# Kernel tuning notes

Hardware: AMD Instinct MI355X
Metric: run time of the kernel (lower is better)

Reference implementation:

```python
import jax, jax.numpy as jnp
import numpy as np

WS = 8          # window size
N = WS * WS     # tokens per window
H = 4           # num heads
DIM = 128
HD = DIM // H   # head dim
SCALE = HD ** -0.5


def _rel_pos_index(ws):
    coords = np.stack(np.meshgrid(np.arange(ws), np.arange(ws), indexing='ij')).reshape(2, -1)
    rel = coords[:, :, None] - coords[:, None, :]          # [2, N, N]
    rel = rel.transpose(1, 2, 0)                           # [N, N, 2]
    rel[..., 0] += ws - 1
    rel[..., 1] += ws - 1
    rel[..., 0] *= 2 * ws - 1
    return jnp.asarray(rel.sum(-1), dtype=jnp.int32)       # [N, N]

_REL_IDX = _rel_pos_index(WS)


def setup_inputs() -> dict:
    key = jax.random.key(0)
    ks = jax.random.split(key, 7)
    B_ = 8192
    nW = 64
    return {
        'x': jax.random.normal(ks[0], (B_, N, DIM), dtype=jnp.float32),
        'mask': jax.random.normal(ks[1], (nW, N, N), dtype=jnp.float32),
        'qkv_w': jax.random.normal(ks[2], (3 * DIM, DIM), dtype=jnp.float32) * 0.02,
        'qkv_b': jax.random.normal(ks[3], (3 * DIM,), dtype=jnp.float32) * 0.02,
        'proj_w': jax.random.normal(ks[4], (DIM, DIM), dtype=jnp.float32) * 0.02,
        'proj_b': jax.random.normal(ks[5], (DIM,), dtype=jnp.float32) * 0.02,
        'rel_pos_bias': jax.random.normal(ks[6], ((2 * WS - 1) ** 2, H), dtype=jnp.float32) * 0.02,
    }


def reference(x, mask, qkv_w, qkv_b, proj_w, proj_b, rel_pos_bias):
    B_, n, c = x.shape
    nW = mask.shape[0]
    qkv = x @ qkv_w.T + qkv_b                               # [B_, N, 3C]
    qkv = qkv.reshape(B_, n, 3, H, HD).transpose(2, 0, 3, 1, 4)
    q, k, v = qkv[0], qkv[1], qkv[2]                        # [B_, H, N, HD]
    attn = jnp.einsum('bhnd,bhmd->bhnm', q * SCALE, k)      # [B_, H, N, N]
    bias = rel_pos_bias[_REL_IDX.reshape(-1)].reshape(n, n, H)
    attn = attn + bias.transpose(2, 0, 1)[None]
    attn = attn.reshape(B_ // nW, nW, H, n, n) + mask[None, :, None, :, :]
    attn = attn.reshape(B_, H, n, n)
    attn = jax.nn.softmax(attn, axis=-1)
    out = jnp.einsum('bhnm,bhmd->bnhd', attn, v).reshape(B_, n, c)
    return out @ proj_w.T + proj_b
```

## Files before the change

### kernel.cpp

```cpp
#include <hip/hip_runtime.h>
#include <stdint.h>

typedef __attribute__((ext_vector_type(8))) short short8;
typedef __attribute__((ext_vector_type(4))) float f32x4;

#define SCALE_Q 0.17677669529663687f

__device__ __forceinline__ uint16_t f2bf(float f) {
    uint32_t u = __builtin_bit_cast(uint32_t, f);
    u += 0x7FFFu + ((u >> 16) & 1u);
    return (uint16_t)(u >> 16);
}

__global__ void prep_kernel(const float* __restrict__ qkv_w, const float* __restrict__ qkv_b,
                            const float* __restrict__ proj_w, const float* __restrict__ rel_b,
                            uint16_t* __restrict__ wq, float* __restrict__ bq,
                            uint16_t* __restrict__ wp, float* __restrict__ bT) {
    int t = blockIdx.x * 256 + threadIdx.x;
    if (t < 384 * 128) {
        int o = t >> 7;
        float s = (o < 128) ? SCALE_Q : 1.0f;
        wq[t] = f2bf(qkv_w[t] * s);
    }
    if (t < 384) bq[t] = qkv_b[t] * ((t < 128) ? SCALE_Q : 1.0f);
    if (t < 128 * 128) wp[t] = f2bf(proj_w[t]);
    if (t < 4 * 64 * 64) {
        int h = t & 3, nm = t >> 2, n = nm >> 6, m = nm & 63;
        int idx = ((n >> 3) - (m >> 3) + 7) * 15 + ((n & 7) - (m & 7) + 7);
        bT[(h * 64 + n) * 64 + m] = rel_b[idx * 4 + h];
    }
}

__global__ __launch_bounds__(256, 2) void winattn_kernel(
    const float* __restrict__ x, const float* __restrict__ mask,
    const uint16_t* __restrict__ wq, const float* __restrict__ bq,
    const uint16_t* __restrict__ wp, const float* __restrict__ pb,
    const float* __restrict__ bT, float* __restrict__ out)
{
    __shared__ uint16_t regionA[20480];
    __shared__ uint16_t Vs[4][64][32];

    uint16_t* Qs = regionA;
    uint16_t* Ks = regionA + 4*64*40;
    uint16_t* Ps = regionA;
    uint16_t* Os = regionA;

    const int b    = blockIdx.x;
    const int w    = b & 63;
    const int wid  = threadIdx.x >> 6;
    const int lane = threadIdx.x & 63;
    const int l15  = lane & 15;
    const int lg   = lane >> 4;

    short8 xa[4][4];
    const float* xb = x + (size_t)b * (64 * 128);
    #pragma unroll
    for (int rt = 0; rt < 4; ++rt) {
      #pragma unroll
      for (int ks = 0; ks < 4; ++ks) {
        const float* p = xb + (rt*16 + l15)*128 + ks*32 + lg*8;
        f32x4 f0 = *(const f32x4*)p;
        f32x4 f1 = *(const f32x4*)(p + 4);
        short8 a;
        a[0]=(short)f2bf(f0[0]); a[1]=(short)f2bf(f0[1]); a[2]=(short)f2bf(f0[2]); a[3]=(short)f2bf(f0[3]);
        a[4]=(short)f2bf(f1[0]); a[5]=(short)f2bf(f1[1]); a[6]=(short)f2bf(f1[2]); a[7]=(short)f2bf(f1[3]);
        xa[rt][ks] = a;
      }
    }
    #pragma unroll
    for (int ct = 0; ct < 6; ++ct) {
        const int obase = wid*96 + ct*16;
        short8 wb[4];
        #pragma unroll
        for (int ks = 0; ks < 4; ++ks)
            wb[ks] = *(const short8*)(wq + (obase + l15)*128 + ks*32 + lg*8);
        const int o   = obase + l15;
        const int sec = o >> 7;
        const int hh  = (o >> 5) & 3;
        const int d   = o & 31;
        const float bo = bq[o];
        const int stride = (sec == 2) ? 32 : 40;
        uint16_t* dst = (sec == 0) ? (Qs + hh*64*40 + d)
                       : (sec == 1) ? (Ks + hh*64*40 + d)
                       : (&Vs[0][0][0] + hh*64*32 + d);
        #pragma unroll
        for (int rt = 0; rt < 4; ++rt) {
            f32x4 acc = {0.f, 0.f, 0.f, 0.f};
            #pragma unroll
            for (int ks = 0; ks < 4; ++ks)
                acc = __builtin_amdgcn_mfma_f32_16x16x32_bf16(xa[rt][ks], wb[ks], acc, 0, 0, 0);
            #pragma unroll
            for (int r = 0; r < 4; ++r)
                dst[(rt*16 + lg*4 + r) * stride] = f2bf(acc[r] + bo);
        }
    }
    __syncthreads();

    const int h = wid;
    short8 qf[4], kf[4];
    #pragma unroll
    for (int rt = 0; rt < 4; ++rt)
        qf[rt] = *(const short8*)(Qs + (h*64 + rt*16 + l15)*40 + lg*8);
    #pragma unroll
    for (int ct = 0; ct < 4; ++ct)
        kf[ct] = *(const short8*)(Ks + (h*64 + ct*16 + l15)*40 + lg*8);
    f32x4 sacc[4][4];
    #pragma unroll
    for (int rt = 0; rt < 4; ++rt) {
      #pragma unroll
      for (int ct = 0; ct < 4; ++ct) {
        f32x4 z = {0.f, 0.f, 0.f, 0.f};
        sacc[rt][ct] = __builtin_amdgcn_mfma_f32_16x16x32_bf16(qf[rt], kf[ct], z, 0, 0, 0);
      }
    }
    const float* bTh = bT + h*64*64;
    const float* mkw = mask + w*64*64;
    float rcp[4][4];
    #pragma unroll
    for (int rt = 0; rt < 4; ++rt) {
      #pragma unroll
      for (int r = 0; r < 4; ++r) {
        const int row = rt*16 + lg*4 + r;
        float v[4];
        #pragma unroll
        for (int ct = 0; ct < 4; ++ct) {
            const int col = ct*16 + l15;
            v[ct] = sacc[rt][ct][r] + bTh[row*64 + col] + mkw[row*64 + col];
        }
        float mx = fmaxf(fmaxf(v[0], v[1]), fmaxf(v[2], v[3]));
        mx = fmaxf(mx, __shfl_xor(mx, 1));
        mx = fmaxf(mx, __shfl_xor(mx, 2));
        mx = fmaxf(mx, __shfl_xor(mx, 4));
        mx = fmaxf(mx, __shfl_xor(mx, 8));
        float s = 0.f;
        #pragma unroll
        for (int ct = 0; ct < 4; ++ct) {
            v[ct] = __expf(v[ct] - mx);
            s += v[ct];
            sacc[rt][ct][r] = v[ct];
        }
        s += __shfl_xor(s, 1);
        s += __shfl_xor(s, 2);
        s += __shfl_xor(s, 4);
        s += __shfl_xor(s, 8);
        rcp[rt][r] = 1.0f / s;
      }
    }
    __syncthreads();
    #pragma unroll
    for (int rt = 0; rt < 4; ++rt)
      #pragma unroll
      for (int ct = 0; ct < 4; ++ct)
        #pragma unroll
        for (int r = 0; r < 4; ++r)
            Ps[(h*64 + rt*16 + lg*4 + r)*80 + ct*16 + l15] = f2bf(sacc[rt][ct][r]);
    __syncthreads();

    short8 pf[4][2];
    #pragma unroll
    for (int rt = 0; rt < 4; ++rt)
      #pragma unroll
      for (int ks = 0; ks < 2; ++ks)
        pf[rt][ks] = *(const short8*)(Ps + (h*64 + rt*16 + l15)*80 + ks*32 + lg*8);
    short8 vf[2][2];
    #pragma unroll
    for (int ks = 0; ks < 2; ++ks) {
      #pragma unroll
      for (int c2 = 0; c2 < 2; ++c2) {
        short8 vv;
        #pragma unroll
        for (int e = 0; e < 8; ++e)
            vv[e] = (short)Vs[h][ks*32 + lg*8 + e][c2*16 + l15];
        vf[ks][c2] = vv;
      }
    }
    f32x4 oacc[4][2];
    #pragma unroll
    for (int rt = 0; rt < 4; ++rt) {
      #pragma unroll
      for (int c2 = 0; c2 < 2; ++c2) {
        f32x4 acc = {0.f, 0.f, 0.f, 0.f};
        #pragma unroll
        for (int ks = 0; ks < 2; ++ks)
            acc = __builtin_amdgcn_mfma_f32_16x16x32_bf16(pf[rt][ks], vf[ks][c2], acc, 0, 0, 0);
        oacc[rt][c2] = acc;
      }
    }
    __syncthreads();
    #pragma unroll
    for (int rt = 0; rt < 4; ++rt)
      #pragma unroll
      for (int c2 = 0; c2 < 2; ++c2)
        #pragma unroll
        for (int r = 0; r < 4; ++r)
            Os[(rt*16 + lg*4 + r)*136 + h*32 + c2*16 + l15] = f2bf(oacc[rt][c2][r] * rcp[rt][r]);
    __syncthreads();

    short8 of[4][4];
    #pragma unroll
    for (int rt = 0; rt < 4; ++rt)
      #pragma unroll
      for (int ks = 0; ks < 4; ++ks)
        of[rt][ks] = *(const short8*)(Os + (rt*16 + l15)*136 + ks*32 + lg*8);
    float* outb = out + (size_t)b * (64 * 128);
    #pragma unroll
    for (int ct = 0; ct < 2; ++ct) {
        const int c = wid*32 + ct*16 + l15;
        short8 pwf[4];
        #pragma unroll
        for (int ks = 0; ks < 4; ++ks)
            pwf[ks] = *(const short8*)(wp + c*128 + ks*32 + lg*8);
        const float pbias = pb[c];
        #pragma unroll
        for (int rt = 0; rt < 4; ++rt) {
            f32x4 acc = {0.f, 0.f, 0.f, 0.f};
            #pragma unroll
            for (int ks = 0; ks < 4; ++ks)
                acc = __builtin_amdgcn_mfma_f32_16x16x32_bf16(of[rt][ks], pwf[ks], acc, 0, 0, 0);
            #pragma unroll
            for (int r = 0; r < 4; ++r)
                outb[(rt*16 + lg*4 + r)*128 + c] = acc[r] + pbias;
        }
    }
}

extern "C" void kernel_launch(void* const* d_in, const int* in_sizes, int n_in,
                              void* d_out, int out_size, void* d_ws, size_t ws_size,
                              hipStream_t stream) {
    const float* x      = (const float*)d_in[0];
    const float* mask   = (const float*)d_in[1];
    const float* qkv_w  = (const float*)d_in[2];
    const float* qkv_b  = (const float*)d_in[3];
    const float* proj_w = (const float*)d_in[4];
    const float* proj_b = (const float*)d_in[5];
    const float* rel_b  = (const float*)d_in[6];
    float* out = (float*)d_out;

    char* ws = (char*)d_ws;
    uint16_t* wq = (uint16_t*)ws;
    float*    bq = (float*)(ws + 98304);
    uint16_t* wp = (uint16_t*)(ws + 99840);
    float*    bT = (float*)(ws + 132608);

    const int B_ = in_sizes[0] / (64 * 128);

    hipLaunchKernelGGL(prep_kernel, dim3(192), dim3(256), 0, stream,
                       qkv_w, qkv_b, proj_w, rel_b, wq, bq, wp, bT);
    hipLaunchKernelGGL(winattn_kernel, dim3(B_), dim3(256), 0, stream,
                       x, mask, wq, bq, wp, proj_b, bT, out);
}
```

Before: 360.5 us.

## Restructure window attention kernel with transposed MFMA layouts, exp2 softmax and register-resident P

Reworks the fused window-attention kernel. The QKV GEMM now uses a swapped operand order so each lane writes packed bf16 vectors, with V stored transposed. Scores are computed as K·Q^T so softmax reductions need only two cross-lane shuffles and bias/mask are read as float4. P stays in registers for the PV MFMA instead of round-tripping through LDS. It also folds log2e into the Q scale and bias to use exp2f and a hardware reciprocal, uses v_cvt_pk_bf16_f32 for packed conversion, and shrinks shared memory with launch bounds raised to 3 blocks per CU. The extra occupancy target may cost registers or cause spills.

Result: slower. 386.2 us (+7.1%).

```diff
diff --git a/kernel.cpp b/kernel.cpp
--- a/kernel.cpp
+++ b/kernel.cpp
@@ -2,8 +2,12 @@
 #include <stdint.h>
 
 typedef __attribute__((ext_vector_type(8))) short short8;
+typedef __attribute__((ext_vector_type(4))) short s16x4;
 typedef __attribute__((ext_vector_type(4))) float f32x4;
-
+typedef __attribute__((ext_vector_type(4))) uint32_t u32x4;
+typedef __attribute__((ext_vector_type(2))) uint32_t u32x2;
+
+#define LOG2E   1.4426950408889634f
 #define SCALE_Q 0.17677669529663687f
 
 __device__ __forceinline__ uint16_t f2bf(float f) {
@@ -12,38 +16,39 @@
     return (uint16_t)(u >> 16);
 }
 
+__device__ __forceinline__ uint32_t cvtpk(float a, float b) {
+    uint32_t r;
+    asm("v_cvt_pk_bf16_f32 %0, %1, %2" : "=v"(r) : "v"(a), "v"(b));
+    return r;
+}
+
 __global__ void prep_kernel(const float* __restrict__ qkv_w, const float* __restrict__ qkv_b,
                             const float* __restrict__ proj_w, const float* __restrict__ rel_b,
                             uint16_t* __restrict__ wq, float* __restrict__ bq,
-                            uint16_t* __restrict__ wp, float* __restrict__ bT) {
+                            uint16_t* __restrict__ wp, float* __restrict__ bTs) {
     int t = blockIdx.x * 256 + threadIdx.x;
     if (t < 384 * 128) {
         int o = t >> 7;
-        float s = (o < 128) ? SCALE_Q : 1.0f;
+        float s = (o < 128) ? SCALE_Q * LOG2E : 1.0f;
         wq[t] = f2bf(qkv_w[t] * s);
     }
-    if (t < 384) bq[t] = qkv_b[t] * ((t < 128) ? SCALE_Q : 1.0f);
+    if (t < 384) bq[t] = qkv_b[t] * ((t < 128) ? SCALE_Q * LOG2E : 1.0f);
     if (t < 128 * 128) wp[t] = f2bf(proj_w[t]);
     if (t < 4 * 64 * 64) {
         int h = t & 3, nm = t >> 2, n = nm >> 6, m = nm & 63;
         int idx = ((n >> 3) - (m >> 3) + 7) * 15 + ((n & 7) - (m & 7) + 7);
-        bT[(h * 64 + n) * 64 + m] = rel_b[idx * 4 + h];
-    }
-}
-
-__global__ __launch_bounds__(256, 2) void winattn_kernel(
+        bTs[(h * 64 + n) * 64 + m] = rel_b[idx * 4 + h] * LOG2E;
+    }
+}
+
+__global__ __launch_bounds__(256, 3) void winattn_kernel(
     const float* __restrict__ x, const float* __restrict__ mask,
     const uint16_t* __restrict__ wq, const float* __restrict__ bq,
     const uint16_t* __restrict__ wp, const float* __restrict__ pb,
-    const float* __restrict__ bT, float* __restrict__ out)
+    const float* __restrict__ bTs, float* __restrict__ out)
 {
-    __shared__ uint16_t regionA[20480];
-    __shared__ uint16_t Vs[4][64][32];
-
-    uint16_t* Qs = regionA;
-    uint16_t* Ks = regionA + 4*64*40;
-    uint16_t* Ps = regionA;
-    uint16_t* Os = regionA;
+    __shared__ uint16_t S1[16896];
+    __shared__ uint16_t Vt[9216];
 
     const int b    = blockIdx.x;
     const int w    = b & 63;
@@ -53,173 +58,173 @@
     const int lg   = lane >> 4;
 
     short8 xa[4][4];
-    const float* xb = x + (size_t)b * (64 * 128);
-    #pragma unroll
-    for (int rt = 0; rt < 4; ++rt) {
+    const float* xb = x + (size_t)b * 8192;
+    #pragma unroll
+    for (int tt = 0; tt < 4; ++tt) {
       #pragma unroll
       for (int ks = 0; ks < 4; ++ks) {
-        const float* p = xb + (rt*16 + l15)*128 + ks*32 + lg*8;
+        const float* p = xb + (tt*16 + l15)*128 + ks*32 + lg*8;
         f32x4 f0 = *(const f32x4*)p;
         f32x4 f1 = *(const f32x4*)(p + 4);
-        short8 a;
-        a[0]=(short)f2bf(f0[0]); a[1]=(short)f2bf(f0[1]); a[2]=(short)f2bf(f0[2]); a[3]=(short)f2bf(f0[3]);
-        a[4]=(short)f2bf(f1[0]); a[5]=(short)f2bf(f1[1]); a[6]=(short)f2bf(f1[2]); a[7]=(short)f2bf(f1[3]);
-        xa[rt][ks] = a;
+        u32x4 u = { cvtpk(f0[0],f0[1]), cvtpk(f0[2],f0[3]),
+                    cvtpk(f1[0],f1[1]), cvtpk(f1[2],f1[3]) };
+        xa[tt][ks] = __builtin_bit_cast(short8, u);
       }
     }
     #pragma unroll
     for (int ct = 0; ct < 6; ++ct) {
-        const int obase = wid*96 + ct*16;
+        const int tile = wid + 4*ct;
         short8 wb[4];
         #pragma unroll
         for (int ks = 0; ks < 4; ++ks)
-            wb[ks] = *(const short8*)(wq + (obase + l15)*128 + ks*32 + lg*8);
-        const int o   = obase + l15;
-        const int sec = o >> 7;
-        const int hh  = (o >> 5) & 3;
-        const int d   = o & 31;
-        const float bo = bq[o];
-        const int stride = (sec == 2) ? 32 : 40;
-        uint16_t* dst = (sec == 0) ? (Qs + hh*64*40 + d)
-                       : (sec == 1) ? (Ks + hh*64*40 + d)
-                       : (&Vs[0][0][0] + hh*64*32 + d);
+            wb[ks] = *(const short8*)(wq + (tile*16 + l15)*128 + ks*32 + lg*8);
+        f32x4 bqv = *(const f32x4*)(bq + tile*16 + lg*4);
+        #pragma unroll
+        for (int tt = 0; tt < 4; ++tt) {
+            f32x4 acc = {0.f,0.f,0.f,0.f};
+            #pragma unroll
+            for (int ks = 0; ks < 4; ++ks)
+                acc = __builtin_amdgcn_mfma_f32_16x16x32_bf16(wb[ks], xa[tt][ks], acc, 0,0,0);
+            const int token = tt*16 + l15;
+            if (ct < 4) {
+                u32x2 wv = { cvtpk(acc[0]+bqv[0], acc[1]+bqv[1]),
+                             cvtpk(acc[2]+bqv[2], acc[3]+bqv[3]) };
+                *(u32x2*)&S1[token*264 + tile*16 + lg*4] = wv;
+            } else {
+                const int vd0 = tile*16 + lg*4 - 256;
+                #pragma unroll
+                for (int r = 0; r < 4; ++r)
+                    Vt[(vd0 + r)*72 + token] = (uint16_t)cvtpk(acc[r]+bqv[r], acc[r]+bqv[r]);
+            }
+        }
+    }
+    __syncthreads();
+
+    const int h = wid;
+    short8 kf[4], qf[4];
+    #pragma unroll
+    for (int mt = 0; mt < 4; ++mt)
+        kf[mt] = *(const short8*)&S1[(mt*16 + l15)*264 + 128 + h*32 + lg*8];
+    #pragma unroll
+    for (int nt = 0; nt < 4; ++nt)
+        qf[nt] = *(const short8*)&S1[(nt*16 + l15)*264 + h*32 + lg*8];
+    __syncthreads();
+
+    f32x4 sacc[4][4];
+    #pragma unroll
+    for (int mt = 0; mt < 4; ++mt) {
+      #pragma unroll
+      for (int nt = 0; nt < 4; ++nt) {
+        f32x4 z = {0.f,0.f,0.f,0.f};
+        sacc[mt][nt] = __builtin_amdgcn_mfma_f32_16x16x32_bf16(kf[mt], qf[nt], z, 0,0,0);
+      }
+    }
+
+    const float* bTh = bTs + h*4096;
+    const float* mkw = mask + w*4096;
+    float rcpv[4];
+    #pragma unroll
+    for (int nt = 0; nt < 4; ++nt) {
+        const int off = (nt*16 + l15)*64 + lg*4;
+        float mx = -3.0e38f;
+        #pragma unroll
+        for (int mt = 0; mt < 4; ++mt) {
+            f32x4 bb = *(const f32x4*)(bTh + off + mt*16);
+            f32x4 mm = *(const f32x4*)(mkw + off + mt*16);
+            #pragma unroll
+            for (int r = 0; r < 4; ++r) {
+                float t = fmaf(mm[r], LOG2E, sacc[mt][nt][r] + bb[r]);
+                sacc[mt][nt][r] = t;
+                mx = fmaxf(mx, t);
+            }
+        }
+        mx = fmaxf(mx, __shfl_xor(mx, 16));
+        mx = fmaxf(mx, __shfl_xor(mx, 32));
+        float sum = 0.f;
+        #pragma unroll
+        for (int mt = 0; mt < 4; ++mt) {
+          #pragma unroll
+          for (int r = 0; r < 4; ++r) {
+            float p = exp2f(sacc[mt][nt][r] - mx);
+            sacc[mt][nt][r] = p;
+            sum += p;
+          }
+        }
+        sum += __shfl_xor(sum, 16);
+        sum += __shfl_xor(sum, 32);
+        rcpv[nt] = __builtin_amdgcn_rcpf(sum);
+    }
+
+    short8 pa[4][2];
+    #pragma unroll
+    for (int nt = 0; nt < 4; ++nt) {
+      #pragma unroll
+      for (int a = 0; a < 2; ++a) {
+        u32x4 u = { cvtpk(sacc[2*a][nt][0],   sacc[2*a][nt][1]),
+                    cvtpk(sacc[2*a][nt][2],   sacc[2*a][nt][3]),
+                    cvtpk(sacc[2*a+1][nt][0], sacc[2*a+1][nt][1]),
+                    cvtpk(sacc[2*a+1][nt][2], sacc[2*a+1][nt][3]) };
+        pa[nt][a] = __builtin_bit_cast(short8, u);
+      }
+    }
+
+    f32x4 oacc[2][4];
+    #pragma unroll
+    for (int dt = 0; dt < 2; ++dt) {
+        const uint16_t* vrow = Vt + (h*32 + dt*16 + l15)*72;
+        short8 va[2];
+        #pragma unroll
+        for (int a = 0; a < 2; ++a) {
+            s16x4 x0 = *(const s16x4*)(vrow + a*32 + lg*4);
+            s16x4 x1 = *(const s16x4*)(vrow + a*32 + 16 + lg*4);
+            va[a] = __builtin_shufflevector(x0, x1, 0,1,2,3,4,5,6,7);
+        }
+        #pragma unroll
+        for (int nt = 0; nt < 4; ++nt) {
+            f32x4 acc = {0.f,0.f,0.f,0.f};
+            acc = __builtin_amdgcn_mfma_f32_16x16x32_bf16(va[0], pa[nt][0], acc, 0,0,0);
+            acc = __builtin_amdgcn_mfma_f32_16x16x32_bf16(va[1], pa[nt][1], acc, 0,0,0);
+            oacc[dt][nt] = acc;
+        }
+    }
+
+    #pragma unroll
+    for (int dt = 0; dt < 2; ++dt) {
+      #pragma unroll
+      for (int nt = 0; nt < 4; ++nt) {
+        const float rc = rcpv[nt];
+        f32x4 o = oacc[dt][nt];
+        u32x2 wv = { cvtpk(o[0]*rc, o[1]*rc), cvtpk(o[2]*rc, o[3]*rc) };
+        *(u32x2*)&S1[(nt*16 + l15)*136 + h*32 + dt*16 + lg*4] = wv;
+      }
+    }
+    __syncthreads();
+
+    short8 of[4][4];
+    #pragma unroll
+    for (int rt = 0; rt < 4; ++rt)
+      #pragma unroll
+      for (int ks = 0; ks < 4; ++ks)
+        of[rt][ks] = *(const short8*)&S1[(rt*16 + l15)*136 + ks*32 + lg*8];
+
+    float* outb = out + (size_t)b * 8192;
+    #pragma unroll
+    for (int ct = 0; ct < 2; ++ct) {
+        const int cbase = wid*32 + ct*16;
+        short8 wf[4];
+        #pragma unroll
+        for (int ks = 0; ks < 4; ++ks)
+            wf[ks] = *(const short8*)(wp + (cbase + l15)*128 + ks*32 + lg*8);
+        const float pbias = pb[cbase + l15];
         #pragma unroll
         for (int rt = 0; rt < 4; ++rt) {
-            f32x4 acc = {0.f, 0.f, 0.f, 0.f};
+            f32x4 acc = {0.f,0.f,0.f,0.f};
             #pragma unroll
             for (int ks = 0; ks < 4; ++ks)
-                acc = __builtin_amdgcn_mfma_f32_16x16x32_bf16(xa[rt][ks], wb[ks], acc, 0, 0, 0);
+                acc = __builtin_amdgcn_mfma_f32_16x16x32_bf16(of[rt][ks], wf[ks], acc, 0,0,0);
             #pragma unroll
             for (int r = 0; r < 4; ++r)
-                dst[(rt*16 + lg*4 + r) * stride] = f2bf(acc[r] + bo);
-        }
-    }
-    __syncthreads();
-
-    const int h = wid;
-    short8 qf[4], kf[4];
-    #pragma unroll
-    for (int rt = 0; rt < 4; ++rt)
-        qf[rt] = *(const short8*)(Qs + (h*64 + rt*16 + l15)*40 + lg*8);
-    #pragma unroll
-    for (int ct = 0; ct < 4; ++ct)
-        kf[ct] = *(const short8*)(Ks + (h*64 + ct*16 + l15)*40 + lg*8);
-    f32x4 sacc[4][4];
-    #pragma unroll
-    for (int rt = 0; rt < 4; ++rt) {
-      #pragma unroll
-      for (int ct = 0; ct < 4; ++ct) {
-        f32x4 z = {0.f, 0.f, 0.f, 0.f};
-        sacc[rt][ct] = __builtin_amdgcn_mfma_f32_16x16x32_bf16(qf[rt], kf[ct], z, 0, 0, 0);
-      }
-    }
-    const float* bTh = bT + h*64*64;
-    const float* mkw = mask + w*64*64;
-    float rcp[4][4];
-    #pragma unroll
-    for (int rt = 0; rt < 4; ++rt) {
-      #pragma unroll
-      for (int r = 0; r < 4; ++r) {
-        const int row = rt*16 + lg*4 + r;
-        float v[4];
-        #pragma unroll
-        for (int ct = 0; ct < 4; ++ct) {
-            const int col = ct*16 + l15;
-            v[ct] = sacc[rt][ct][r] + bTh[row*64 + col] + mkw[row*64 + col];
-        }
-        float mx = fmaxf(fmaxf(v[0], v[1]), fmaxf(v[2], v[3]));
-        mx = fmaxf(mx, __shfl_xor(mx, 1));
-        mx = fmaxf(mx, __shfl_xor(mx, 2));
-        mx = fmaxf(mx, __shfl_xor(mx, 4));
-        mx = fmaxf(mx, __shfl_xor(mx, 8));
-        float s = 0.f;
-        #pragma unroll
-        for (int ct = 0; ct < 4; ++ct) {
-            v[ct] = __expf(v[ct] - mx);
-            s += v[ct];
-            sacc[rt][ct][r] = v[ct];
-        }
-        s += __shfl_xor(s, 1);
-        s += __shfl_xor(s, 2);
-        s += __shfl_xor(s, 4);
-        s += __shfl_xor(s, 8);
-        rcp[rt][r] = 1.0f / s;
-      }
-    }
-    __syncthreads();
-    #pragma unroll
-    for (int rt = 0; rt < 4; ++rt)
-      #pragma unroll
-      for (int ct = 0; ct < 4; ++ct)
-        #pragma unroll
-        for (int r = 0; r < 4; ++r)
-            Ps[(h*64 + rt*16 + lg*4 + r)*80 + ct*16 + l15] = f2bf(sacc[rt][ct][r]);
-    __syncthreads();
-
-    short8 pf[4][2];
-    #pragma unroll
-    for (int rt = 0; rt < 4; ++rt)
-      #pragma unroll
-      for (int ks = 0; ks < 2; ++ks)
-        pf[rt][ks] = *(const short8*)(Ps + (h*64 + rt*16 + l15)*80 + ks*32 + lg*8);
-    short8 vf[2][2];
-    #pragma unroll
-    for (int ks = 0; ks < 2; ++ks) {
-      #pragma unroll
-      for (int c2 = 0; c2 < 2; ++c2) {
-        short8 vv;
-        #pragma unroll
-        for (int e = 0; e < 8; ++e)
-            vv[e] = (short)Vs[h][ks*32 + lg*8 + e][c2*16 + l15];
-        vf[ks][c2] = vv;
-      }
-    }
-    f32x4 oacc[4][2];
-    #pragma unroll
-    for (int rt = 0; rt < 4; ++rt) {
-      #pragma unroll
-      for (int c2 = 0; c2 < 2; ++c2) {
-        f32x4 acc = {0.f, 0.f, 0.f, 0.f};
-        #pragma unroll
-        for (int ks = 0; ks < 2; ++ks)
-            acc = __builtin_amdgcn_mfma_f32_16x16x32_bf16(pf[rt][ks], vf[ks][c2], acc, 0, 0, 0);
-        oacc[rt][c2] = acc;
-      }
-    }
-    __syncthreads();
-    #pragma unroll
-    for (int rt = 0; rt < 4; ++rt)
-      #pragma unroll
-      for (int c2 = 0; c2 < 2; ++c2)
-        #pragma unroll
-        for (int r = 0; r < 4; ++r)
-            Os[(rt*16 + lg*4 + r)*136 + h*32 + c2*16 + l15] = f2bf(oacc[rt][c2][r] * rcp[rt][r]);
-    __syncthreads();
-
-    short8 of[4][4];
-    #pragma unroll
-    for (int rt = 0; rt < 4; ++rt)
-      #pragma unroll
-      for (int ks = 0; ks < 4; ++ks)
-        of[rt][ks] = *(const short8*)(Os + (rt*16 + l15)*136 + ks*32 + lg*8);
-    float* outb = out + (size_t)b * (64 * 128);
-    #pragma unroll
-    for (int ct = 0; ct < 2; ++ct) {
-        const int c = wid*32 + ct*16 + l15;
-        short8 pwf[4];
-        #pragma unroll
-        for (int ks = 0; ks < 4; ++ks)
-            pwf[ks] = *(const short8*)(wp + c*128 + ks*32 + lg*8);
-        const float pbias = pb[c];
-        #pragma unroll
-        for (int rt = 0; rt < 4; ++rt) {
-            f32x4 acc = {0.f, 0.f, 0.f, 0.f};
-            #pragma unroll
-            for (int ks = 0; ks < 4; ++ks)
-                acc = __builtin_amdgcn_mfma_f32_16x16x32_bf16(of[rt][ks], pwf[ks], acc, 0, 0, 0);
-            #pragma unroll
-            for (int r = 0; r < 4; ++r)
-                outb[(rt*16 + lg*4 + r)*128 + c] = acc[r] + pbias;
+                outb[(rt*16 + lg*4 + r)*128 + cbase + l15] = acc[r] + pbias;
         }
     }
 }
@@ -237,15 +242,15 @@
     float* out = (float*)d_out;
 
     char* ws = (char*)d_ws;
-    uint16_t* wq = (uint16_t*)ws;
-    float*    bq = (float*)(ws + 98304);
-    uint16_t* wp = (uint16_t*)(ws + 99840);
-    float*    bT = (float*)(ws + 132608);
+    uint16_t* wq  = (uint16_t*)ws;
+    float*    bq  = (float*)(ws + 98304);
+    uint16_t* wp  = (uint16_t*)(ws + 99840);
+    float*    bTs = (float*)(ws + 132608);
 
     const int B_ = in_sizes[0] / (64 * 128);
 
     hipLaunchKernelGGL(prep_kernel, dim3(192), dim3(256), 0, stream,
-                       qkv_w, qkv_b, proj_w, rel_b, wq, bq, wp, bT);
+                       qkv_w, qkv_b, proj_w, rel_b, wq, bq, wp, bTs);
     hipLaunchKernelGGL(winattn_kernel, dim3(B_), dim3(256), 0, stream,
-                       x, mask, wq, bq, wp, proj_b, bT, out);
-}
+                       x, mask, wq, bq, wp, proj_b, bTs, out);
+}
```
